# Kernel tuning notes

Measured on AMD Instinct MI355X. Metric: run time of the kernel, lower is better.

Reference implementation:

```python
import jax, jax.numpy as jnp
import numpy as np

N_M, N_D, N_A = 100000, 30000, 80000


def setup_inputs() -> dict:
    key = jax.random.key(0)
    ks = jax.random.split(key, 24)
    d_in, d_h, d_out = 64, 64, 32
    inp = {
        "x_movie": jax.random.normal(ks[0], (N_M, d_in), jnp.float32),
        "x_director": jax.random.normal(ks[1], (N_D, d_in), jnp.float32),
        "x_actor": jax.random.normal(ks[2], (N_A, d_in), jnp.float32),
        "src_md": jax.random.randint(ks[3], (1500000,), 0, N_M, jnp.int32),
        "dst_md": jax.random.randint(ks[4], (1500000,), 0, N_D, jnp.int32),
        "ew_md": jax.random.uniform(ks[5], (1500000,), jnp.float32),
        "src_dm": jax.random.randint(ks[6], (1500000,), 0, N_D, jnp.int32),
        "dst_dm": jax.random.randint(ks[7], (1500000,), 0, N_M, jnp.int32),
        "ew_dm": jax.random.uniform(ks[8], (1500000,), jnp.float32),
        "src_ma": jax.random.randint(ks[9], (2000000,), 0, N_M, jnp.int32),
        "dst_ma": jax.random.randint(ks[10], (2000000,), 0, N_A, jnp.int32),
        "ew_ma": jax.random.uniform(ks[11], (2000000,), jnp.float32),
        "src_am": jax.random.randint(ks[12], (2000000,), 0, N_A, jnp.int32),
        "dst_am": jax.random.randint(ks[13], (2000000,), 0, N_M, jnp.int32),
        "ew_am": jax.random.uniform(ks[14], (2000000,), jnp.float32),
        "W1_rel": jax.random.normal(ks[15], (4, d_in, d_h), jnp.float32) * 0.05,
        "b1": jax.random.normal(ks[16], (4, d_h), jnp.float32) * 0.05,
        "W1_root": jax.random.normal(ks[17], (4, d_in, d_h), jnp.float32) * 0.05,
        "W2_rel": jax.random.normal(ks[18], (4, d_h, d_out), jnp.float32) * 0.05,
        "b2": jax.random.normal(ks[19], (4, d_out), jnp.float32) * 0.05,
        "W2_root": jax.random.normal(ks[20], (4, d_h, d_out), jnp.float32) * 0.05,
    }
    return inp


def _hetero_layer(x_m, x_d, x_a, edges, ews, W_rel, b, W_root):
    # relation order: 0 = movie->director, 1 = director->movie,
    #                 2 = movie->actor,    3 = actor->movie
    (src_md, dst_md, src_dm, dst_dm, src_ma, dst_ma, src_am, dst_am) = edges
    (ew_md, ew_dm, ew_ma, ew_am) = ews
    # GraphConv: aggregate edge-weighted source features, then linear.
    agg_md = jax.ops.segment_sum(x_m[src_md] * ew_md[:, None], dst_md, num_segments=N_D)
    agg_dm = jax.ops.segment_sum(x_d[src_dm] * ew_dm[:, None], dst_dm, num_segments=N_M)
    agg_ma = jax.ops.segment_sum(x_m[src_ma] * ew_ma[:, None], dst_ma, num_segments=N_A)
    agg_am = jax.ops.segment_sum(x_a[src_am] * ew_am[:, None], dst_am, num_segments=N_M)
    out_d = agg_md @ W_rel[0] + b[0] + x_d @ W_root[0]
    out_m = (agg_dm @ W_rel[1] + b[1] + x_m @ W_root[1]) \
          + (agg_am @ W_rel[3] + b[3] + x_m @ W_root[3])  # HeteroConv aggr='sum'
    out_a = agg_ma @ W_rel[2] + b[2] + x_a @ W_root[2]
    return out_m, out_d, out_a


def reference(x_movie, x_director, x_actor,
              src_md, dst_md, ew_md, src_dm, dst_dm, ew_dm,
              src_ma, dst_ma, ew_ma, src_am, dst_am, ew_am,
              W1_rel, b1, W1_root, W2_rel, b2, W2_root):
    edges = (src_md, dst_md, src_dm, dst_dm, src_ma, dst_ma, src_am, dst_am)
    ews = (ew_md, ew_dm, ew_ma, ew_am)
    h_m, h_d, h_a = _hetero_layer(x_movie, x_director, x_actor, edges, ews, W1_rel, b1, W1_root)
    h_m, h_d, h_a = jax.nn.relu(h_m), jax.nn.relu(h_d), jax.nn.relu(h_a)
    o_m, o_d, o_a = _hetero_layer(h_m, h_d, h_a, edges, ews, W2_rel, b2, W2_root)
    return o_m, o_d, o_a
```

## Files before the change

kernel.cpp:

```cpp
#include <hip/hip_runtime.h>

#define N_M 100000
#define N_D 30000
#define N_A 80000

#define CSHIFT 14
#define NC_M 7
#define NC_D 2
#define NC_A 5

#define BO_MD 0
#define BO_DM (BO_MD + N_D * NC_M)
#define BO_MA (BO_DM + N_M * NC_D)
#define BO_AM (BO_MA + N_A * NC_M)
#define B_TOT (BO_AM + N_M * NC_A)

#define FBITS 12
#define NFINE 4096
#define NBUCK ((B_TOT + NFINE - 1) / NFINE)
#define T_A 4096

typedef unsigned int u32;
typedef unsigned short u16;
typedef unsigned long long u64;

__device__ __forceinline__ u16 f2bf(float f) {
  u32 u = __float_as_uint(f);
  return (u16)((u + 0x7FFFu + ((u >> 16) & 1u)) >> 16);
}
__device__ __forceinline__ float bf2f(u16 b) {
  return __uint_as_float(((u32)b) << 16);
}
__device__ __forceinline__ float bf2f_hi(u32 v) {
  return __uint_as_float(v & 0xFFFF0000u);
}
__device__ __forceinline__ u32 pack_edge(int src, float ew) {
  return ((u32)src << 15) | ((u32)f2bf(ew) & 0x7FFFu);
}

struct Rel { const int* src; const int* dst; const float* ew; int nE; int binBase; int nC; };
struct Rel4 { Rel r[4]; int blkStart[5]; };

__global__ __launch_bounds__(256) void phase0(Rel4 P, int* __restrict__ bucketHist) {
  __shared__ u32 lh[512];
  int tid = threadIdx.x;
  int b = blockIdx.x, s = 0;
  while (b >= P.blkStart[s + 1]) s++;
  const Rel R = P.r[s];
  int base = (b - P.blkStart[s]) * T_A;
  for (int i = tid; i < 512; i += 256) lh[i] = 0;
  __syncthreads();
#pragma unroll 4
  for (int k = 0; k < 16; k++) {
    int e = base + tid + k * 256;
    if (e < R.nE) {
      int key = R.binBase + R.dst[e] * R.nC + (R.src[e] >> CSHIFT);
      atomicAdd(&lh[key >> FBITS], 1u);
    }
  }
  __syncthreads();
  for (int i = tid; i < 512; i += 256) if (lh[i]) atomicAdd(&bucketHist[i], (int)lh[i]);
}

__global__ __launch_bounds__(256) void scan_bucket(const int* __restrict__ bucketHist,
                                                   int* __restrict__ bucketBase,
                                                   int* __restrict__ cursor) {
  __shared__ int wsum[4];
  int tid = threadIdx.x;
  int j0 = tid * 2;
  int a0 = (j0 < NBUCK) ? bucketHist[j0] : 0;
  int a1 = (j0 + 1 < NBUCK) ? bucketHist[j0 + 1] : 0;
  int ssum = a0 + a1;
  int lane = tid & 63, wid = tid >> 6;
  int sc = ssum;
#pragma unroll
  for (int off = 1; off < 64; off <<= 1) { int t = __shfl_up(sc, off, 64); if (lane >= off) sc += t; }
  if (lane == 63) wsum[wid] = sc;
  __syncthreads();
  int wex = 0, tot = 0;
  for (int w = 0; w < 4; w++) { int t = wsum[w]; if (w < wid) wex += t; tot += t; }
  int ex = wex + sc - ssum;
  if (j0 < NBUCK) { bucketBase[j0] = ex; cursor[j0] = ex; }
  if (j0 + 1 < NBUCK) { bucketBase[j0 + 1] = ex + a0; cursor[j0 + 1] = ex + a0; }
  if (tid == 0) bucketBase[NBUCK] = tot;
}

__global__ __launch_bounds__(256) void phaseA(Rel4 P, int* __restrict__ cursor,
                                              u64* __restrict__ tmp) {
  __shared__ u32 hist[512], lstart[512], cur[512], gbase[512];
  __shared__ u64 stage[T_A];
  __shared__ u32 wsum[4];
  int tid = threadIdx.x;
  int b = blockIdx.x, s = 0;
  while (b >= P.blkStart[s + 1]) s++;
  const Rel R = P.r[s];
  int base = (b - P.blkStart[s]) * T_A;
  int valid = min(T_A, R.nE - base);
  for (int i = tid; i < 512; i += 256) hist[i] = 0;
  __syncthreads();
#pragma unroll 4
  for (int k = 0; k < 16; k++) {
    int e = base + tid + k * 256;
    if (e < R.nE) {
      int key = R.binBase + R.dst[e] * R.nC + (R.src[e] >> CSHIFT);
      atomicAdd(&hist[key >> FBITS], 1u);
    }
  }
  __syncthreads();
  int c0 = tid * 2;
  u32 h0 = hist[c0], h1 = hist[c0 + 1];
  u32 ssum = h0 + h1;
  int lane = tid & 63, wid = tid >> 6;
  u32 sc = ssum;
#pragma unroll
  for (int off = 1; off < 64; off <<= 1) { int t = __shfl_up((int)sc, off, 64); if (lane >= off) sc += (u32)t; }
  if (lane == 63) wsum[wid] = sc;
  __syncthreads();
  u32 wex = 0;
  for (int w = 0; w < 4; w++) if (w < wid) wex += wsum[w];
  u32 ex = wex + sc - ssum;
  lstart[c0] = ex;       cur[c0] = ex;
  lstart[c0 + 1] = ex + h0; cur[c0 + 1] = ex + h0;
  if (h0) gbase[c0] = (u32)atomicAdd(&cursor[c0], (int)h0);
  if (h1) gbase[c0 + 1] = (u32)atomicAdd(&cursor[c0 + 1], (int)h1);
  __syncthreads();
#pragma unroll 4
  for (int k = 0; k < 16; k++) {
    int e = base + tid + k * 256;
    if (e < R.nE) {
      int srcv = R.src[e];
      int key = R.binBase + R.dst[e] * R.nC + (srcv >> CSHIFT);
      u32 slot = atomicAdd(&cur[key >> FBITS], 1u);
      stage[slot] = ((u64)(u32)key << 32) | pack_edge(srcv, R.ew[e]);
    }
  }
  __syncthreads();
  for (int i = tid; i < valid; i += 256) {
    u64 v = stage[i];
    u32 c = (u32)(v >> (32 + FBITS));
    tmp[gbase[c] + ((u32)i - lstart[c])] = v;
  }
}

__global__ __launch_bounds__(1024) void phaseB(const u64* __restrict__ tmp,
                                               const int* __restrict__ bucketBase,
                                               u32* __restrict__ pairs,
                                               int* __restrict__ bins) {
  __shared__ u32 h2[NFINE], cur2[NFINE];
  __shared__ u32 wsum[16];
  int c = blockIdx.x, tid = threadIdx.x;
  int s0 = bucketBase[c], s1 = bucketBase[c + 1];
  for (int i = tid; i < NFINE; i += 1024) h2[i] = 0;
  __syncthreads();
  for (int e = s0 + tid; e < s1; e += 1024) {
    u32 fine = (u32)(tmp[e] >> 32) & (NFINE - 1);
    atomicAdd(&h2[fine], 1u);
  }
  __syncthreads();
  int f0 = tid * 4;
  u32 v[4], ssum = 0;
#pragma unroll
  for (int i = 0; i < 4; i++) { v[i] = h2[f0 + i]; ssum += v[i]; }
  int lane = tid & 63, wid = tid >> 6;
  u32 sc = ssum;
#pragma unroll
  for (int off = 1; off < 64; off <<= 1) { int t = __shfl_up((int)sc, off, 64); if (lane >= off) sc += (u32)t; }
  if (lane == 63) wsum[wid] = sc;
  __syncthreads();
  u32 wex = 0;
#pragma unroll
  for (int w = 0; w < 16; w++) if (w < wid) wex += wsum[w];
  u32 ex = wex + sc - ssum;
  int binBase0 = c << FBITS;
#pragma unroll
  for (int i = 0; i < 4; i++) {
    int gb = binBase0 + f0 + i;
    if (gb < B_TOT) bins[gb] = s0 + (int)ex;
    cur2[f0 + i] = ex;
    ex += v[i];
  }
  if (c == NBUCK - 1 && tid == 0) bins[B_TOT] = s1;
  __syncthreads();
  for (int e = s0 + tid; e < s1; e += 1024) {
    u64 t = tmp[e];
    u32 fine = (u32)(t >> 32) & (NFINE - 1);
    u32 pos = atomicAdd(&cur2[fine], 1u);
    pairs[s0 + pos] = (u32)t;
  }
}

__global__ __launch_bounds__(256) void l1_tr_m(
    const float* __restrict__ x,
    const float* __restrict__ Wr0, const float* __restrict__ Wr2,
    const float* __restrict__ Wt1, const float* __restrict__ Wt3,
    const float* __restrict__ b1a, const float* __restrict__ b1b,
    u16* __restrict__ t0, u16* __restrict__ t2, u16* __restrict__ r, int n) {
  __shared__ float A[4096], B[4096], C[4096];
  for (int i = threadIdx.x * 4; i < 4096; i += 1024) {
    *(float4*)&A[i] = *(const float4*)&Wr0[i];
    *(float4*)&B[i] = *(const float4*)&Wr2[i];
    float4 p = *(const float4*)&Wt1[i], q = *(const float4*)&Wt3[i];
    *(float4*)&C[i] = make_float4(p.x + q.x, p.y + q.y, p.z + q.z, p.w + q.w);
  }
  __syncthreads();
  int lane = threadIdx.x & 63, wid = threadIdx.x >> 6;
  int wave = blockIdx.x * 4 + wid, nW = gridDim.x * 4;
  float bj = b1a[lane] + b1b[lane];
  for (int base = wave * 4; base < n; base += nW * 4) {
    int n0 = base, n1 = min(base + 1, n - 1), n2 = min(base + 2, n - 1), n3 = min(base + 3, n - 1);
    float o0a = 0, o0b = 0, o0c = bj, o1a = 0, o1b = 0, o1c = bj;
    float o2a = 0, o2b = 0, o2c = bj, o3a = 0, o3b = 0, o3c = bj;
#pragma unroll 4
    for (int k = 0; k < 64; k++) {
      float wa = A[k * 64 + lane], wb = B[k * 64 + lane], wc = C[k * 64 + lane];
      float x0 = x[(size_t)n0 * 64 + k], x1 = x[(size_t)n1 * 64 + k];
      float x2 = x[(size_t)n2 * 64 + k], x3 = x[(size_t)n3 * 64 + k];
      o0a = fmaf(x0, wa, o0a); o0b = fmaf(x0, wb, o0b); o0c = fmaf(x0, wc, o0c);
      o1a = fmaf(x1, wa, o1a); o1b = fmaf(x1, wb, o1b); o1c = fmaf(x1, wc, o1c);
      o2a = fmaf(x2, wa, o2a); o2b = fmaf(x2, wb, o2b); o2c = fmaf(x2, wc, o2c);
      o3a = fmaf(x3, wa, o3a); o3b = fmaf(x3, wb, o3b); o3c = fmaf(x3, wc, o3c);
    }
    t0[(size_t)n0 * 64 + lane] = f2bf(o0a); t2[(size_t)n0 * 64 + lane] = f2bf(o0b); r[(size_t)n0 * 64 + lane] = f2bf(o0c);
    if (base + 1 < n) { t0[(size_t)n1 * 64 + lane] = f2bf(o1a); t2[(size_t)n1 * 64 + lane] = f2bf(o1b); r[(size_t)n1 * 64 + lane] = f2bf(o1c); }
    if (base + 2 < n) { t0[(size_t)n2 * 64 + lane] = f2bf(o2a); t2[(size_t)n2 * 64 + lane] = f2bf(o2b); r[(size_t)n2 * 64 + lane] = f2bf(o2c); }
    if (base + 3 < n) { t0[(size_t)n3 * 64 + lane] = f2bf(o3a); t2[(size_t)n3 * 64 + lane] = f2bf(o3b); r[(size_t)n3 * 64 + lane] = f2bf(o3c); }
  }
}

__global__ __launch_bounds__(256) void l1_tr_s2(
    const float* __restrict__ x1, const float* __restrict__ Wrel1,
    const float* __restrict__ Wroot1, const float* __restrict__ bias1,
    u16* __restrict__ t1o, u16* __restrict__ r1o, int n1, int nBlk1,
    const float* __restrict__ x2, const float* __restrict__ Wrel2,
    const float* __restrict__ Wroot2, const float* __restrict__ bias2,
    u16* __restrict__ t2o, u16* __restrict__ r2o, int n2) {
  __shared__ float A[4096], C[4096];
  bool first = (int)blockIdx.x < nBlk1;
  const float* x = first ? x1 : x2;
  const float* Wrel = first ? Wrel1 : Wrel2;
  const float* Wroot = first ? Wroot1 : Wroot2;
  const float* bias = first ? bias1 : bias2;
  u16* t = first ? t1o : t2o;
  u16* r = first ? r1o : r2o;
  int n = first ? n1 : n2;
  int blk = first ? blockIdx.x : blockIdx.x - nBlk1;
  int nBlk = first ? nBlk1 : (gridDim.x - nBlk1);
  for (int i = threadIdx.x * 4; i < 4096; i += 1024) {
    *(float4*)&A[i] = *(const float4*)&Wrel[i];
    *(float4*)&C[i] = *(const float4*)&Wroot[i];
  }
  __syncthreads();
  int lane = threadIdx.x & 63, wid = threadIdx.x >> 6;
  int wave = blk * 4 + wid, nW = nBlk * 4;
  float bj = bias[lane];
  for (int base = wave * 4; base < n; base += nW * 4) {
    int n0 = base, n1_ = min(base + 1, n - 1), n2_ = min(base + 2, n - 1), n3_ = min(base + 3, n - 1);
    float o0a = 0, o0c = bj, o1a = 0, o1c = bj, o2a = 0, o2c = bj, o3a = 0, o3c = bj;
#pragma unroll 4
    for (int k = 0; k < 64; k++) {
      float wa = A[k * 64 + lane], wc = C[k * 64 + lane];
      float x0 = x[(size_t)n0 * 64 + k], xx1 = x[(size_t)n1_ * 64 + k];
      float xx2 = x[(size_t)n2_ * 64 + k], xx3 = x[(size_t)n3_ * 64 + k];
      o0a = fmaf(x0, wa, o0a); o0c = fmaf(x0, wc, o0c);
      o1a = fmaf(xx1, wa, o1a); o1c = fmaf(xx1, wc, o1c);
      o2a = fmaf(xx2, wa, o2a); o2c = fmaf(xx2, wc, o2c);
      o3a = fmaf(xx3, wa, o3a); o3c = fmaf(xx3, wc, o3c);
    }
    t[(size_t)n0 * 64 + lane] = f2bf(o0a); r[(size_t)n0 * 64 + lane] = f2bf(o0c);
    if (base + 1 < n) { t[(size_t)n1_ * 64 + lane] = f2bf(o1a); r[(size_t)n1_ * 64 + lane] = f2bf(o1c); }
    if (base + 2 < n) { t[(size_t)n2_ * 64 + lane] = f2bf(o2a); r[(size_t)n2_ * 64 + lane] = f2bf(o2c); }
    if (base + 3 < n) { t[(size_t)n3_ * 64 + lane] = f2bf(o3a); r[(size_t)n3_ * 64 + lane] = f2bf(o3c); }
  }
}

__device__ __forceinline__ void g2_pair(u32 pa, u32 pb,
    const u16* __restrict__ tbl, u32 lanebyte, u32 hm,
    float& a0, float& a1) {
  u32 offa = (pa >> 15) << 7, offd = ((pb >> 15) << 7) - offa;
  u32 wa = (pa & 0x7FFFu) << 16, wd = ((pb & 0x7FFFu) << 16) ^ wa;
  u32 v = *(const u32*)((const char*)tbl + ((hm & offd) + offa + lanebyte));
  float w = __uint_as_float((hm & wd) ^ wa);
  a0 = fmaf(w, bf2f((u16)v), a0);
  a1 = fmaf(w, bf2f_hi(v), a1);
}

__device__ __forceinline__ void g2y_pair(u32 pa, u32 pb,
    const u16* __restrict__ tbl, const u16* __restrict__ ytbl,
    u32 lanebyte, u32 ylanebyte, u32 hm,
    float& a0, float& a1, float& ay) {
  u32 ra = pa >> 15, rb = pb >> 15;
  u32 offa = ra << 7, offd = (rb << 7) - offa;
  u32 yoa = ra << 6,  yod = (rb << 6) - yoa;
  u32 wa = (pa & 0x7FFFu) << 16, wd = ((pb & 0x7FFFu) << 16) ^ wa;
  u32 v = *(const u32*)((const char*)tbl + ((hm & offd) + offa + lanebyte));
  u16 q = *(const u16*)((const char*)ytbl + ((hm & yod) + yoa + ylanebyte));
  float w = __uint_as_float((hm & wd) ^ wa);
  a0 = fmaf(w, bf2f((u16)v), a0);
  a1 = fmaf(w, bf2f_hi(v), a1);
  ay = fmaf(w, bf2f(q), ay);
}

#define RL(x, i) ((u32)__builtin_amdgcn_readlane((int)(x), (i)))

__device__ __forceinline__ void gather2_seg64(
    int s0, int s1, const u32* __restrict__ pairs,
    const u16* __restrict__ tbl, u32 lanebyte, u32 hm, int lane, u32 pw0,
    float& a0, float& a1) {
  int base = s0;
  u32 pw = pw0;
  for (;;) {
    int cnt = s1 - base; if (cnt > 64) cnt = 64;
    int e = 0;
    for (; e + 8 <= cnt; e += 8) {
      u32 p0 = RL(pw, e),     p1 = RL(pw, e + 1), p2 = RL(pw, e + 2), p3 = RL(pw, e + 3);
      u32 p4 = RL(pw, e + 4), p5 = RL(pw, e + 5), p6 = RL(pw, e + 6), p7 = RL(pw, e + 7);
      g2_pair(p0, p1, tbl, lanebyte, hm, a0, a1);
      g2_pair(p2, p3, tbl, lanebyte, hm, a0, a1);
      g2_pair(p4, p5, tbl, lanebyte, hm, a0, a1);
      g2_pair(p6, p7, tbl, lanebyte, hm, a0, a1);
    }
    if (e + 4 <= cnt) {
      u32 p0 = RL(pw, e), p1 = RL(pw, e + 1), p2 = RL(pw, e + 2), p3 = RL(pw, e + 3);
      g2_pair(p0, p1, tbl, lanebyte, hm, a0, a1);
      g2_pair(p2, p3, tbl, lanebyte, hm, a0, a1);
      e += 4;
    }
    if (e + 2 <= cnt) {
      u32 p0 = RL(pw, e), p1 = RL(pw, e + 1);
      g2_pair(p0, p1, tbl, lanebyte, hm, a0, a1);
      e += 2;
    }
    if (e < cnt) {
      u32 p = RL(pw, e);
      g2_pair(p, p & 0xFFFF8000u, tbl, lanebyte, hm, a0, a1);
    }
    base += 64;
    if (base >= s1) break;
    pw = (base + lane < s1) ? pairs[base + lane] : 0u;
  }
}

__device__ __forceinline__ void gather2y_seg64(
    int s0, int s1, const u32* __restrict__ pairs,
    const u16* __restrict__ tbl, const u16* __restrict__ ytbl,
    u32 lanebyte, u32 ylanebyte, u32 hm, int lane, u32 pw0,
    float& a0, float& a1, float& ay) {
  int base = s0;
  u32 pw = pw0;
  for (;;) {
    int cnt = s1 - base; if (cnt > 64) cnt = 64;
    int e = 0;
    for (; e + 8 <= cnt; e += 8) {
      u32 p0 = RL(pw, e),     p1 = RL(pw, e + 1), p2 = RL(pw, e + 2), p3 = RL(pw, e + 3);
      u32 p4 = RL(pw, e + 4), p5 = RL(pw, e + 5), p6 = RL(pw, e + 6), p7 = RL(pw, e + 7);
      g2y_pair(p0, p1, tbl, ytbl, lanebyte, ylanebyte, hm, a0, a1, ay);
      g2y_pair(p2, p3, tbl, ytbl, lanebyte, ylanebyte, hm, a0, a1, ay);
      g2y_pair(p4, p5, tbl, ytbl, lanebyte, ylanebyte, hm, a0, a1, ay);
      g2y_pair(p6, p7, tbl, ytbl, lanebyte, ylanebyte, hm, a0, a1, ay);
    }
    if (e + 4 <= cnt) {
      u32 p0 = RL(pw, e), p1 = RL(pw, e + 1), p2 = RL(pw, e + 2), p3 = RL(pw, e + 3);
      g2y_pair(p0, p1, tbl, ytbl, lanebyte, ylanebyte, hm, a0, a1, ay);
      g2y_pair(p2, p3, tbl, ytbl, lanebyte, ylanebyte, hm, a0, a1, ay);
      e += 4;
    }
    if (e + 2 <= cnt) {
      u32 p0 = RL(pw, e), p1 = RL(pw, e + 1);
      g2y_pair(p0, p1, tbl, ytbl, lanebyte, ylanebyte, hm, a0, a1, ay);
      e += 2;
    }
    if (e < cnt) {
      u32 p = RL(pw, e);
      g2y_pair(p, p & 0xFFFF8000u, tbl, ytbl, lanebyte, ylanebyte, hm, a0, a1, ay);
    }
    base += 64;
    if (base >= s1) break;
    pw = (base + lane < s1) ? pairs[base + lane] : 0u;
  }
}

__device__ __forceinline__ void gathero_32(
    int s0, int s1, const u32* __restrict__ pairs,
    const u16* __restrict__ ytbl, int lanebyte, int oaddr, int lane,
    float& a0, float& a1, float& a2, float& a3) {
  for (int base = s0; base < s1; base += 64) {
    u32 pw = 0;
    if (base + lane < s1) pw = pairs[base + lane];
    int ng = min(s1 - base, 64);
    ng = (ng + 7) >> 3;
#pragma unroll 2
    for (int g = 0; g < ng; g++) {
      u32 p = (u32)__builtin_amdgcn_ds_bpermute(oaddr + (g << 5), (int)pw);
      u32 off = ((p >> 15) << 6) + lanebyte;
      float w = __uint_as_float((p & 0x7FFFu) << 16);
      uint2 v = *(const uint2*)((const char*)ytbl + off);
      a0 = fmaf(w, bf2f((u16)v.x), a0);
      a1 = fmaf(w, bf2f_hi(v.x), a1);
      a2 = fmaf(w, bf2f((u16)v.y), a2);
      a3 = fmaf(w, bf2f_hi(v.y), a3);
    }
  }
}

struct F1Side {
  const u16 *tbl, *ytbl, *r1;
  const float *W2r, *W2t, *b2;
  u16 *y; float *out;
  int n, nC, binBase;
};

__global__ __launch_bounds__(512) void fused1(
    const int* __restrict__ bins, const u32* __restrict__ pairs,
    F1Side D, F1Side A, int nBlkD) {
  __shared__ float Wy[2048], Wt[2048];
  __shared__ float bs[32];
  __shared__ __align__(16) float scr[8][64];
  bool isD = (int)blockIdx.x < nBlkD;
  F1Side S = isD ? D : A;
  int blk = isD ? blockIdx.x : blockIdx.x - nBlkD;
  for (int i = threadIdx.x; i < 2048; i += 512) { Wy[i] = S.W2r[i]; Wt[i] = S.W2t[i]; }
  if (threadIdx.x < 32) bs[threadIdx.x] = S.b2[threadIdx.x];
  __syncthreads();
  int lane = threadIdx.x & 63, wid = threadIdx.x >> 6;
  int j = lane & 31, half = lane >> 5;
  u32 lanebyte = (u32)j << 2;
  u32 ylanebyte = (u32)j << 1;
  u32 hm = half ? 0xFFFFFFFFu : 0u;
  int node0 = (blk * 8 + wid) * 8;
  int bnd = bins[S.binBase + min(node0 + min(lane, 8), S.n) * S.nC];
  float acc0[8], acc1[8], accy[8];
#pragma unroll
  for (int i = 0; i < 8; i++) { acc0[i] = 0.f; acc1[i] = 0.f; accy[i] = 0.f; }
  u32 pwp[8];
#pragma unroll
  for (int i = 0; i < 8; i++) {
    int s0 = __builtin_amdgcn_readlane(bnd, i);
    int s1 = __builtin_amdgcn_readlane(bnd, i + 1);
    pwp[i] = (node0 + i < S.n && s0 + lane < s1) ? pairs[s0 + lane] : 0u;
  }
#pragma unroll
  for (int i = 0; i < 8; i++) {
    int s0 = __builtin_amdgcn_readlane(bnd, i);
    int s1 = __builtin_amdgcn_readlane(bnd, i + 1);
    if (node0 + i < S.n && s0 < s1)
      gather2y_seg64(s0, s1, pairs, S.tbl, S.ytbl, lanebyte, ylanebyte, hm, lane, pwp[i],
                     acc0[i], acc1[i], accy[i]);
  }
#pragma unroll
  for (int i = 0; i < 8; i++) {
    int node = node0 + i;
    if (node >= S.n) continue;
    float a0 = acc0[i] + __shfl_xor(acc0[i], 32);
    float a1 = acc1[i] + __shfl_xor(acc1[i], 32);
    float ayt = accy[i] + __shfl_xor(accy[i], 32);
    u32 rv = *(const u32*)&S.r1[(size_t)node * 64 + 2 * j];
    float hv0 = fmaxf(a0 + bf2f((u16)rv), 0.f);
    float hv1 = fmaxf(a1 + bf2f_hi(rv), 0.f);
    if (!half) *(float2*)&scr[wid][2 * j] = make_float2(hv0, hv1);
    float oy = 0.f, ot = 0.f;
#pragma unroll
    for (int kk = 0; kk < 32; kk++) {
      int k = (half << 5) + kk;
      float s = scr[wid][k];
      oy = fmaf(s, Wy[k * 32 + j], oy);
      ot = fmaf(s, Wt[k * 32 + j], ot);
    }
    oy += __shfl_xor(oy, 32);
    ot += __shfl_xor(ot, 32);
    if (lane < 32) {
      S.y[(size_t)node * 32 + lane] = f2bf(oy);
      S.out[(size_t)node * 32 + lane] = ot + bs[lane] + ayt;
    }
  }
}

__global__ __launch_bounds__(512) void fusedm(
    const int* __restrict__ bins, const u32* __restrict__ pairs,
    const u16* __restrict__ tbl1,
    const u16* __restrict__ tbl2,
    const u16* __restrict__ r1,
    const float* __restrict__ W2r0, const float* __restrict__ W2r2,
    const float* __restrict__ W2t1, const float* __restrict__ W2t3,
    const float* __restrict__ b2a, const float* __restrict__ b2b,
    u16* __restrict__ y0, u16* __restrict__ y2, float* __restrict__ oroot, int n) {
  __shared__ float Wy0[2048], Wy2[2048], Wt[2048];
  __shared__ float bs[32];
  __shared__ __align__(16) float scr[8][64];
  for (int i = threadIdx.x; i < 2048; i += 512) {
    Wy0[i] = W2r0[i]; Wy2[i] = W2r2[i]; Wt[i] = W2t1[i] + W2t3[i];
  }
  if (threadIdx.x < 32) bs[threadIdx.x] = b2a[threadIdx.x] + b2b[threadIdx.x];
  __syncthreads();
  int lane = threadIdx.x & 63, wid = threadIdx.x >> 6;
  int j = lane & 31, half = lane >> 5;
  u32 lanebyte = (u32)j << 2;
  u32 hm = half ? 0xFFFFFFFFu : 0u;
  int node0 = (blockIdx.x * 8 + wid) * 8;
  int bdm = bins[BO_DM + min(node0 + min(lane, 8), n) * NC_D];
  int bam = bins[BO_AM + min(node0 + min(lane, 8), n) * NC_A];
  float acc0[8], acc1[8];
#pragma unroll
  for (int i = 0; i < 8; i++) { acc0[i] = 0.f; acc1[i] = 0.f; }
  {
    u32 pwp[8];
#pragma unroll
    for (int i = 0; i < 8; i++) {
      int s0 = __builtin_amdgcn_readlane(bdm, i);
      int s1 = __builtin_amdgcn_readlane(bdm, i + 1);
      pwp[i] = (node0 + i < n && s0 + lane < s1) ? pairs[s0 + lane] : 0u;
    }
#pragma unroll
    for (int i = 0; i < 8; i++) {
      int s0 = __builtin_amdgcn_readlane(bdm, i);
      int s1 = __builtin_amdgcn_readlane(bdm, i + 1);
      if (node0 + i < n && s0 < s1)
        gather2_seg64(s0, s1, pairs, tbl1, lanebyte, hm, lane, pwp[i], acc0[i], acc1[i]);
    }
  }
  {
    u32 pwp[8];
#pragma unroll
    for (int i = 0; i < 8; i++) {
      int s0 = __builtin_amdgcn_readlane(bam, i);
      int s1 = __builtin_amdgcn_readlane(bam, i + 1);
      pwp[i] = (node0 + i < n && s0 + lane < s1) ? pairs[s0 + lane] : 0u;
    }
#pragma unroll
    for (int i = 0; i < 8; i++) {
      int s0 = __builtin_amdgcn_readlane(bam, i);
      int s1 = __builtin_amdgcn_readlane(bam, i + 1);
      if (node0 + i < n && s0 < s1)
        gather2_seg64(s0, s1, pairs, tbl2, lanebyte, hm, lane, pwp[i], acc0[i], acc1[i]);
    }
  }
#pragma unroll
  for (int i = 0; i < 8; i++) {
    int node = node0 + i;
    if (node >= n) continue;
    float a0 = acc0[i] + __shfl_xor(acc0[i], 32);
    float a1 = acc1[i] + __shfl_xor(acc1[i], 32);
    u32 rv = *(const u32*)&r1[(size_t)node * 64 + 2 * j];
    float hv0 = fmaxf(a0 + bf2f((u16)rv), 0.f);
    float hv1 = fmaxf(a1 + bf2f_hi(rv), 0.f);
    if (!half) *(float2*)&scr[wid][2 * j] = make_float2(hv0, hv1);
    float o0 = 0.f, o2 = 0.f, ot = 0.f;
#pragma unroll
    for (int kk = 0; kk < 32; kk++) {
      int k = (half << 5) + kk;
      float s = scr[wid][k];
      o0 = fmaf(s, Wy0[k * 32 + j], o0);
      o2 = fmaf(s, Wy2[k * 32 + j], o2);
      ot = fmaf(s, Wt[k * 32 + j], ot);
    }
    o0 += __shfl_xor(o0, 32);
    o2 += __shfl_xor(o2, 32);
    ot += __shfl_xor(ot, 32);
    if (lane < 32) {
      y0[(size_t)node * 32 + lane] = f2bf(o0);
      y2[(size_t)node * 32 + lane] = f2bf(o2);
      oroot[(size_t)node * 32 + lane] = ot + bs[lane];
    }
  }
}

__global__ __launch_bounds__(256) void outm(
    const int* __restrict__ bins, const u32* __restrict__ pairs,
    const u16* __restrict__ y1,
    const u16* __restrict__ y2,
    float* __restrict__ out, int n) {
  int lane = threadIdx.x & 63, wid = threadIdx.x >> 6;
  int node0 = (blockIdx.x * 4 + wid) * 8;
  int j8 = lane & 7;
  int lanebyte = j8 << 3;
  int oaddr = (lane >> 3) << 2;
  int bdm = bins[BO_DM + min(node0 + min(lane, 8), n) * NC_D];
  int bam = bins[BO_AM + min(node0 + min(lane, 8), n) * NC_A];
  float acc0[8], acc1[8], acc2[8], acc3[8];
#pragma unroll
  for (int i = 0; i < 8; i++) { acc0[i] = 0.f; acc1[i] = 0.f; acc2[i] = 0.f; acc3[i] = 0.f; }
#pragma unroll
  for (int i = 0; i < 8; i++) {
    int s0 = __builtin_amdgcn_readlane(bdm, i);
    int s1 = __builtin_amdgcn_readlane(bdm, i + 1);
    if (node0 + i < n) gathero_32(s0, s1, pairs, y1, lanebyte, oaddr, lane,
                                  acc0[i], acc1[i], acc2[i], acc3[i]);
  }
#pragma unroll
  for (int i = 0; i < 8; i++) {
    int s0 = __builtin_amdgcn_readlane(bam, i);
    int s1 = __builtin_amdgcn_readlane(bam, i + 1);
    if (node0 + i < n) gathero_32(s0, s1, pairs, y2, lanebyte, oaddr, lane,
                                  acc0[i], acc1[i], acc2[i], acc3[i]);
  }
#pragma unroll
  for (int i = 0; i < 8; i++) {
    int node = node0 + i;
    if (node >= n) continue;
    float a0 = acc0[i], a1 = acc1[i], a2 = acc2[i], a3 = acc3[i];
    a0 += __shfl_xor(a0, 8); a0 += __shfl_xor(a0, 16); a0 += __shfl_xor(a0, 32);
    a1 += __shfl_xor(a1, 8); a1 += __shfl_xor(a1, 16); a1 += __shfl_xor(a1, 32);
    a2 += __shfl_xor(a2, 8); a2 += __shfl_xor(a2, 16); a2 += __shfl_xor(a2, 32);
    a3 += __shfl_xor(a3, 8); a3 += __shfl_xor(a3, 16); a3 += __shfl_xor(a3, 32);
    if (lane < 8) {
      float4* o = (float4*)((char*)out + (size_t)node * 128 + (j8 << 4));
      float4 v = *o;
      v.x += a0; v.y += a1; v.z += a2; v.w += a3;
      *o = v;
    }
  }
}

static inline int nblkA(long long e) { return (int)((e + T_A - 1) / T_A); }

extern "C" void kernel_launch(void* const* d_in, const int* in_sizes, int n_in,
                              void* d_out, int out_size, void* d_ws, size_t ws_size,
                              hipStream_t stream) {
  const float* x_m = (const float*)d_in[0];
  const float* x_d = (const float*)d_in[1];
  const float* x_a = (const float*)d_in[2];
  const int* src_md = (const int*)d_in[3];
  const int* dst_md = (const int*)d_in[4];
  const float* ew_md = (const float*)d_in[5];
  const int* src_dm = (const int*)d_in[6];
  const int* dst_dm = (const int*)d_in[7];
  const float* ew_dm = (const float*)d_in[8];
  const int* src_ma = (const int*)d_in[9];
  const int* dst_ma = (const int*)d_in[10];
  const float* ew_ma = (const float*)d_in[11];
  const int* src_am = (const int*)d_in[12];
  const int* dst_am = (const int*)d_in[13];
  const float* ew_am = (const float*)d_in[14];
  const float* W1_rel = (const float*)d_in[15];
  const float* b1 = (const float*)d_in[16];
  const float* W1_root = (const float*)d_in[17];
  const float* W2_rel = (const float*)d_in[18];
  const float* b2 = (const float*)d_in[19];
  const float* W2_root = (const float*)d_in[20];

  const int E_md = in_sizes[3];
  const int E_dm = in_sizes[6];
  const int E_ma = in_sizes[9];
  const int E_am = in_sizes[12];
  const long long E_tot = (long long)E_md + E_dm + E_ma + E_am;

  char* w = (char*)d_ws;
  u64* tmp = (u64*)w;       w += (size_t)E_tot * 8;
  u32* pairs = (u32*)w;     w += (size_t)E_tot * 4;
  int* bins = (int*)w;      w += (size_t)(B_TOT + 1) * 4;
  int* bucketHist = (int*)w; w += 512 * 4;
  int* bucketBase = (int*)w; w += (NBUCK + 1) * 4;
  int* cursor = (int*)w;     w += 512 * 4;
  u16* r_d  = (u16*)w;      w += (size_t)N_D * 64 * 2;
  u16* r_a  = (u16*)w;      w += (size_t)N_A * 64 * 2;
  u16* y_md = (u16*)w;      w += (size_t)N_M * 32 * 2;
  u16* y_dm = (u16*)w;      w += (size_t)N_D * 32 * 2;
  u16* y_ma = (u16*)w;      w += (size_t)N_M * 32 * 2;
  u16* y_am = (u16*)w;      w += (size_t)N_A * 32 * 2;
  if ((size_t)(w - (char*)d_ws) > ws_size) return;
  char* ta = (char*)tmp;
  u16* t_md = (u16*)ta;     ta += (size_t)N_M * 64 * 2;
  u16* t_dm = (u16*)ta;     ta += (size_t)N_D * 64 * 2;
  u16* t_ma = (u16*)ta;     ta += (size_t)N_M * 64 * 2;
  u16* t_am = (u16*)ta;     ta += (size_t)N_A * 64 * 2;
  u16* r_m  = (u16*)ta;     ta += (size_t)N_M * 64 * 2;

  float* o_m = (float*)d_out;
  float* o_d = o_m + (size_t)N_M * 32;
  float* o_a = o_d + (size_t)N_D * 32;

  hipMemsetAsync(bucketHist, 0, 512 * 4, stream);

  Rel4 P;
  P.r[0] = { src_md, dst_md, ew_md, E_md, BO_MD, NC_M };
  P.r[1] = { src_dm, dst_dm, ew_dm, E_dm, BO_DM, NC_D };
  P.r[2] = { src_ma, dst_ma, ew_ma, E_ma, BO_MA, NC_M };
  P.r[3] = { src_am, dst_am, ew_am, E_am, BO_AM, NC_A };
  P.blkStart[0] = 0;
  P.blkStart[1] = P.blkStart[0] + nblkA(E_md);
  P.blkStart[2] = P.blkStart[1] + nblkA(E_dm);
  P.blkStart[3] = P.blkStart[2] + nblkA(E_ma);
  P.blkStart[4] = P.blkStart[3] + nblkA(E_am);

  phase0<<<P.blkStart[4], 256, 0, stream>>>(P, bucketHist);
  scan_bucket<<<1, 256, 0, stream>>>(bucketHist, bucketBase, cursor);
  phaseA<<<P.blkStart[4], 256, 0, stream>>>(P, cursor, tmp);
  phaseB<<<NBUCK, 1024, 0, stream>>>(tmp, bucketBase, pairs, bins);

  l1_tr_m<<<768, 256, 0, stream>>>(x_m, W1_rel + 0 * 4096, W1_rel + 2 * 4096,
                                   W1_root + 1 * 4096, W1_root + 3 * 4096,
                                   b1 + 1 * 64, b1 + 3 * 64, t_md, t_ma, r_m, N_M);
  l1_tr_s2<<<1024, 256, 0, stream>>>(
      x_d, W1_rel + 1 * 4096, W1_root + 0 * 4096, b1 + 0 * 64, t_dm, r_d, N_D, 512,
      x_a, W1_rel + 3 * 4096, W1_root + 2 * 4096, b1 + 2 * 64, t_am, r_a, N_A);

  fusedm<<<(N_M + 63) / 64, 512, 0, stream>>>(bins, pairs, t_dm, t_am, r_m,
      W2_rel + 0 * 2048, W2_rel + 2 * 2048, W2_root + 1 * 2048, W2_root + 3 * 2048,
      b2 + 1 * 32, b2 + 3 * 32, y_md, y_ma, o_m, N_M);

  int nBlkD = (N_D + 63) / 64;
  int nBlkA_ = (N_A + 63) / 64;
  F1Side Dside = { t_md, y_md, r_d, W2_rel + 1 * 2048, W2_root + 0 * 2048, b2 + 0 * 32,
                   y_dm, o_d, N_D, NC_M, BO_MD };
  F1Side Aside = { t_ma, y_ma, r_a, W2_rel + 3 * 2048, W2_root + 2 * 2048, b2 + 2 * 32,
                   y_am, o_a, N_A, NC_M, BO_MA };
  fused1<<<nBlkD + nBlkA_, 512, 0, stream>>>(bins, pairs, Dside, Aside, nBlkD);

  outm<<<(N_M + 31) / 32, 256, 0, stream>>>(bins, pairs, y_dm, y_am, o_m, N_M);
}
```

Baseline: 850.4 us.

## Replace two-level radix sort CSR build with atomic counting sort by destination

Swaps the bucketed two-pass radix sort, which ordered edges by destination and source chunk, for a simple counting sort: per-destination degree histogram via global atomics, a single-block scan, then an atomic scatter into CSR. This drops the 64-bit temp buffer pass and the source-chunk ordering. The cost is heavy global atomic contention, a serial single-block scan over about 310k bins, a nondeterministic order within each bin, and the loss of source locality in later gathers.

```diff
diff --git a/kernel.cpp b/kernel.cpp
--- a/kernel.cpp
+++ b/kernel.cpp
@@ -4,20 +4,12 @@
 #define N_D 30000
 #define N_A 80000
 
-#define CSHIFT 14
-#define NC_M 7
-#define NC_D 2
-#define NC_A 5
-
-#define BO_MD 0
-#define BO_DM (BO_MD + N_D * NC_M)
-#define BO_MA (BO_DM + N_M * NC_D)
-#define BO_AM (BO_MA + N_A * NC_M)
-#define B_TOT (BO_AM + N_M * NC_A)
-
-#define FBITS 12
-#define NFINE 4096
-#define NBUCK ((B_TOT + NFINE - 1) / NFINE)
+#define B2_MD 0
+#define B2_DM (N_D)
+#define B2_MA (N_D + N_M)
+#define B2_AM (N_D + N_M + N_A)
+#define B2_TOT (N_D + 2 * N_M + N_A)
+
 #define T_A 4096
 
 typedef unsigned int u32;
@@ -38,154 +30,62 @@
   return ((u32)src << 15) | ((u32)f2bf(ew) & 0x7FFFu);
 }
 
-struct Rel { const int* src; const int* dst; const float* ew; int nE; int binBase; int nC; };
+struct Rel { const int* src; const int* dst; const float* ew; int nE; int binBase; };
 struct Rel4 { Rel r[4]; int blkStart[5]; };
 
-__global__ __launch_bounds__(256) void phase0(Rel4 P, int* __restrict__ bucketHist) {
-  __shared__ u32 lh[512];
-  int tid = threadIdx.x;
+__global__ __launch_bounds__(256) void count_deg(Rel4 P, int* __restrict__ hist) {
   int b = blockIdx.x, s = 0;
   while (b >= P.blkStart[s + 1]) s++;
   const Rel R = P.r[s];
   int base = (b - P.blkStart[s]) * T_A;
-  for (int i = tid; i < 512; i += 256) lh[i] = 0;
+  int tid = threadIdx.x;
+#pragma unroll 4
+  for (int k = 0; k < 16; k++) {
+    int e = base + tid + k * 256;
+    if (e < R.nE) atomicAdd(&hist[R.binBase + R.dst[e]], 1);
+  }
+}
+
+__global__ __launch_bounds__(1024) void scan_bins(int* __restrict__ cursor,
+                                                  int* __restrict__ bins) {
+  __shared__ int wsum[16];
+  int tid = threadIdx.x;
+  const int CH = (B2_TOT + 1023) / 1024;
+  int lo = tid * CH, hi = min(lo + CH, B2_TOT);
+  int s = 0;
+  for (int i = lo; i < hi; i++) s += cursor[i];
+  int lane = tid & 63, wid = tid >> 6;
+  int sc = s;
+#pragma unroll
+  for (int off = 1; off < 64; off <<= 1) { int t = __shfl_up(sc, off, 64); if (lane >= off) sc += t; }
+  if (lane == 63) wsum[wid] = sc;
   __syncthreads();
+  int wex = 0;
+#pragma unroll
+  for (int w = 0; w < 16; w++) if (w < wid) wex += wsum[w];
+  int run = wex + sc - s;
+  for (int i = lo; i < hi; i++) {
+    int v = cursor[i];
+    bins[i] = run; cursor[i] = run;
+    run += v;
+  }
+  if (tid == 1023) bins[B2_TOT] = run;
+}
+
+__global__ __launch_bounds__(256) void scatter(Rel4 P, int* __restrict__ cursor,
+                                               u32* __restrict__ pairs) {
+  int b = blockIdx.x, s = 0;
+  while (b >= P.blkStart[s + 1]) s++;
+  const Rel R = P.r[s];
+  int base = (b - P.blkStart[s]) * T_A;
+  int tid = threadIdx.x;
 #pragma unroll 4
   for (int k = 0; k < 16; k++) {
     int e = base + tid + k * 256;
     if (e < R.nE) {
-      int key = R.binBase + R.dst[e] * R.nC + (R.src[e] >> CSHIFT);
-      atomicAdd(&lh[key >> FBITS], 1u);
-    }
-  }
-  __syncthreads();
-  for (int i = tid; i < 512; i += 256) if (lh[i]) atomicAdd(&bucketHist[i], (int)lh[i]);
-}
-
-__global__ __launch_bounds__(256) void scan_bucket(const int* __restrict__ bucketHist,
-                                                   int* __restrict__ bucketBase,
-                                                   int* __restrict__ cursor) {
-  __shared__ int wsum[4];
-  int tid = threadIdx.x;
-  int j0 = tid * 2;
-  int a0 = (j0 < NBUCK) ? bucketHist[j0] : 0;
-  int a1 = (j0 + 1 < NBUCK) ? bucketHist[j0 + 1] : 0;
-  int ssum = a0 + a1;
-  int lane = tid & 63, wid = tid >> 6;
-  int sc = ssum;
-#pragma unroll
-  for (int off = 1; off < 64; off <<= 1) { int t = __shfl_up(sc, off, 64); if (lane >= off) sc += t; }
-  if (lane == 63) wsum[wid] = sc;
-  __syncthreads();
-  int wex = 0, tot = 0;
-  for (int w = 0; w < 4; w++) { int t = wsum[w]; if (w < wid) wex += t; tot += t; }
-  int ex = wex + sc - ssum;
-  if (j0 < NBUCK) { bucketBase[j0] = ex; cursor[j0] = ex; }
-  if (j0 + 1 < NBUCK) { bucketBase[j0 + 1] = ex + a0; cursor[j0 + 1] = ex + a0; }
-  if (tid == 0) bucketBase[NBUCK] = tot;
-}
-
-__global__ __launch_bounds__(256) void phaseA(Rel4 P, int* __restrict__ cursor,
-                                              u64* __restrict__ tmp) {
-  __shared__ u32 hist[512], lstart[512], cur[512], gbase[512];
-  __shared__ u64 stage[T_A];
-  __shared__ u32 wsum[4];
-  int tid = threadIdx.x;
-  int b = blockIdx.x, s = 0;
-  while (b >= P.blkStart[s + 1]) s++;
-  const Rel R = P.r[s];
-  int base = (b - P.blkStart[s]) * T_A;
-  int valid = min(T_A, R.nE - base);
-  for (int i = tid; i < 512; i += 256) hist[i] = 0;
-  __syncthreads();
-#pragma unroll 4
-  for (int k = 0; k < 16; k++) {
-    int e = base + tid + k * 256;
-    if (e < R.nE) {
-      int key = R.binBase + R.dst[e] * R.nC + (R.src[e] >> CSHIFT);
-      atomicAdd(&hist[key >> FBITS], 1u);
-    }
-  }
-  __syncthreads();
-  int c0 = tid * 2;
-  u32 h0 = hist[c0], h1 = hist[c0 + 1];
-  u32 ssum = h0 + h1;
-  int lane = tid & 63, wid = tid >> 6;
-  u32 sc = ssum;
-#pragma unroll
-  for (int off = 1; off < 64; off <<= 1) { int t = __shfl_up((int)sc, off, 64); if (lane >= off) sc += (u32)t; }
-  if (lane == 63) wsum[wid] = sc;
-  __syncthreads();
-  u32 wex = 0;
-  for (int w = 0; w < 4; w++) if (w < wid) wex += wsum[w];
-  u32 ex = wex + sc - ssum;
-  lstart[c0] = ex;       cur[c0] = ex;
-  lstart[c0 + 1] = ex + h0; cur[c0 + 1] = ex + h0;
-  if (h0) gbase[c0] = (u32)atomicAdd(&cursor[c0], (int)h0);
-  if (h1) gbase[c0 + 1] = (u32)atomicAdd(&cursor[c0 + 1], (int)h1);
-  __syncthreads();
-#pragma unroll 4
-  for (int k = 0; k < 16; k++) {
-    int e = base + tid + k * 256;
-    if (e < R.nE) {
-      int srcv = R.src[e];
-      int key = R.binBase + R.dst[e] * R.nC + (srcv >> CSHIFT);
-      u32 slot = atomicAdd(&cur[key >> FBITS], 1u);
-      stage[slot] = ((u64)(u32)key << 32) | pack_edge(srcv, R.ew[e]);
-    }
-  }
-  __syncthreads();
-  for (int i = tid; i < valid; i += 256) {
-    u64 v = stage[i];
-    u32 c = (u32)(v >> (32 + FBITS));
-    tmp[gbase[c] + ((u32)i - lstart[c])] = v;
-  }
-}
-
-__global__ __launch_bounds__(1024) void phaseB(const u64* __restrict__ tmp,
-                                               const int* __restrict__ bucketBase,
-                                               u32* __restrict__ pairs,
-                                               int* __restrict__ bins) {
-  __shared__ u32 h2[NFINE], cur2[NFINE];
-  __shared__ u32 wsum[16];
-  int c = blockIdx.x, tid = threadIdx.x;
-  int s0 = bucketBase[c], s1 = bucketBase[c + 1];
-  for (int i = tid; i < NFINE; i += 1024) h2[i] = 0;
-  __syncthreads();
-  for (int e = s0 + tid; e < s1; e += 1024) {
-    u32 fine = (u32)(tmp[e] >> 32) & (NFINE - 1);
-    atomicAdd(&h2[fine], 1u);
-  }
-  __syncthreads();
-  int f0 = tid * 4;
-  u32 v[4], ssum = 0;
-#pragma unroll
-  for (int i = 0; i < 4; i++) { v[i] = h2[f0 + i]; ssum += v[i]; }
-  int lane = tid & 63, wid = tid >> 6;
-  u32 sc = ssum;
-#pragma unroll
-  for (int off = 1; off < 64; off <<= 1) { int t = __shfl_up((int)sc, off, 64); if (lane >= off) sc += (u32)t; }
-  if (lane == 63) wsum[wid] = sc;
-  __syncthreads();
-  u32 wex = 0;
-#pragma unroll
-  for (int w = 0; w < 16; w++) if (w < wid) wex += wsum[w];
-  u32 ex = wex + sc - ssum;
-  int binBase0 = c << FBITS;
-#pragma unroll
-  for (int i = 0; i < 4; i++) {
-    int gb = binBase0 + f0 + i;
-    if (gb < B_TOT) bins[gb] = s0 + (int)ex;
-    cur2[f0 + i] = ex;
-    ex += v[i];
-  }
-  if (c == NBUCK - 1 && tid == 0) bins[B_TOT] = s1;
-  __syncthreads();
-  for (int e = s0 + tid; e < s1; e += 1024) {
-    u64 t = tmp[e];
-    u32 fine = (u32)(t >> 32) & (NFINE - 1);
-    u32 pos = atomicAdd(&cur2[fine], 1u);
-    pairs[s0 + pos] = (u32)t;
+      int pos = atomicAdd(&cursor[R.binBase + R.dst[e]], 1);
+      pairs[pos] = pack_edge(R.src[e], R.ew[e]);
+    }
   }
 }
 
@@ -406,7 +306,7 @@
   const u16 *tbl, *ytbl, *r1;
   const float *W2r, *W2t, *b2;
   u16 *y; float *out;
-  int n, nC, binBase;
+  int n, binBase;
 };
 
 __global__ __launch_bounds__(512) void fused1(
@@ -427,7 +327,7 @@
   u32 ylanebyte = (u32)j << 1;
   u32 hm = half ? 0xFFFFFFFFu : 0u;
   int node0 = (blk * 8 + wid) * 8;
-  int bnd = bins[S.binBase + min(node0 + min(lane, 8), S.n) * S.nC];
+  int bnd = bins[S.binBase + min(node0 + min(lane, 8), S.n)];
   float acc0[8], acc1[8], accy[8];
 #pragma unroll
   for (int i = 0; i < 8; i++) { acc0[i] = 0.f; acc1[i] = 0.f; accy[i] = 0.f; }
@@ -496,8 +396,8 @@
   u32 lanebyte = (u32)j << 2;
   u32 hm = half ? 0xFFFFFFFFu : 0u;
   int node0 = (blockIdx.x * 8 + wid) * 8;
-  int bdm = bins[BO_DM + min(node0 + min(lane, 8), n) * NC_D];
-  int bam = bins[BO_AM + min(node0 + min(lane, 8), n) * NC_A];
+  int bdm = bins[B2_DM + min(node0 + min(lane, 8), n)];
+  int bam = bins[B2_AM + min(node0 + min(lane, 8), n)];
   float acc0[8], acc1[8];
 #pragma unroll
   for (int i = 0; i < 8; i++) { acc0[i] = 0.f; acc1[i] = 0.f; }
@@ -573,8 +473,8 @@
   int j8 = lane & 7;
   int lanebyte = j8 << 3;
   int oaddr = (lane >> 3) << 2;
-  int bdm = bins[BO_DM + min(node0 + min(lane, 8), n) * NC_D];
-  int bam = bins[BO_AM + min(node0 + min(lane, 8), n) * NC_A];
+  int bdm = bins[B2_DM + min(node0 + min(lane, 8), n)];
+  int bam = bins[B2_AM + min(node0 + min(lane, 8), n)];
   float acc0[8], acc1[8], acc2[8], acc3[8];
 #pragma unroll
   for (int i = 0; i < 8; i++) { acc0[i] = 0.f; acc1[i] = 0.f; acc2[i] = 0.f; acc3[i] = 0.f; }
@@ -646,10 +546,8 @@
   char* w = (char*)d_ws;
   u64* tmp = (u64*)w;       w += (size_t)E_tot * 8;
   u32* pairs = (u32*)w;     w += (size_t)E_tot * 4;
-  int* bins = (int*)w;      w += (size_t)(B_TOT + 1) * 4;
-  int* bucketHist = (int*)w; w += 512 * 4;
-  int* bucketBase = (int*)w; w += (NBUCK + 1) * 4;
-  int* cursor = (int*)w;     w += 512 * 4;
+  int* bins = (int*)w;      w += (size_t)(B2_TOT + 1) * 4;
+  int* cursor = (int*)w;    w += (size_t)B2_TOT * 4;
   u16* r_d  = (u16*)w;      w += (size_t)N_D * 64 * 2;
   u16* r_a  = (u16*)w;      w += (size_t)N_A * 64 * 2;
   u16* y_md = (u16*)w;      w += (size_t)N_M * 32 * 2;
@@ -668,23 +566,22 @@
   float* o_d = o_m + (size_t)N_M * 32;
   float* o_a = o_d + (size_t)N_D * 32;
 
-  hipMemsetAsync(bucketHist, 0, 512 * 4, stream);
+  hipMemsetAsync(cursor, 0, (size_t)B2_TOT * 4, stream);
 
   Rel4 P;
-  P.r[0] = { src_md, dst_md, ew_md, E_md, BO_MD, NC_M };
-  P.r[1] = { src_dm, dst_dm, ew_dm, E_dm, BO_DM, NC_D };
-  P.r[2] = { src_ma, dst_ma, ew_ma, E_ma, BO_MA, NC_M };
-  P.r[3] = { src_am, dst_am, ew_am, E_am, BO_AM, NC_A };
+  P.r[0] = { src_md, dst_md, ew_md, E_md, B2_MD };
+  P.r[1] = { src_dm, dst_dm, ew_dm, E_dm, B2_DM };
+  P.r[2] = { src_ma, dst_ma, ew_ma, E_ma, B2_MA };
+  P.r[3] = { src_am, dst_am, ew_am, E_am, B2_AM };
   P.blkStart[0] = 0;
   P.blkStart[1] = P.blkStart[0] + nblkA(E_md);
   P.blkStart[2] = P.blkStart[1] + nblkA(E_dm);
   P.blkStart[3] = P.blkStart[2] + nblkA(E_ma);
   P.blkStart[4] = P.blkStart[3] + nblkA(E_am);
 
-  phase0<<<P.blkStart[4], 256, 0, stream>>>(P, bucketHist);
-  scan_bucket<<<1, 256, 0, stream>>>(bucketHist, bucketBase, cursor);
-  phaseA<<<P.blkStart[4], 256, 0, stream>>>(P, cursor, tmp);
-  phaseB<<<NBUCK, 1024, 0, stream>>>(tmp, bucketBase, pairs, bins);
+  count_deg<<<P.blkStart[4], 256, 0, stream>>>(P, cursor);
+  scan_bins<<<1, 1024, 0, stream>>>(cursor, bins);
+  scatter<<<P.blkStart[4], 256, 0, stream>>>(P, cursor, pairs);
 
   l1_tr_m<<<768, 256, 0, stream>>>(x_m, W1_rel + 0 * 4096, W1_rel + 2 * 4096,
                                    W1_root + 1 * 4096, W1_root + 3 * 4096,
@@ -700,9 +597,9 @@
   int nBlkD = (N_D + 63) / 64;
   int nBlkA_ = (N_A + 63) / 64;
   F1Side Dside = { t_md, y_md, r_d, W2_rel + 1 * 2048, W2_root + 0 * 2048, b2 + 0 * 32,
-                   y_dm, o_d, N_D, NC_M, BO_MD };
+                   y_dm, o_d, N_D, B2_MD };
   F1Side Aside = { t_ma, y_ma, r_a, W2_rel + 3 * 2048, W2_root + 2 * 2048, b2 + 2 * 32,
-                   y_am, o_a, N_A, NC_M, BO_MA };
+                   y_am, o_a, N_A, B2_MA };
   fused1<<<nBlkD + nBlkA_, 512, 0, stream>>>(bins, pairs, Dside, Aside, nBlkD);
 
   outm<<<(N_M + 31) / 32, 256, 0, stream>>>(bins, pairs, y_dm, y_am, o_m, N_M);
```

Result: slower. 1.973 ms (+132.0%).
